# Kernel tuning notes

Hardware: AMD Instinct MI355X
Metric: run time of the kernel (lower is better)

The kernel has to match this reference:

```python
import jax, jax.numpy as jnp
import numpy as np
from jax import lax

REPLACE_PROB = 0.12
B, I, T = 16, 256, 8192


def setup_inputs() -> dict:
    key = jax.random.key(0)
    p = REPLACE_PROB
    s = 1.0 - 2.0 * p
    # probs[p2, p1, :] = P(x_t | x_{t-2}=p2, x_{t-1}=p1); all rows [p, s, p]
    # except [2,1] which disallows jitter value 0 (the '012' triplet) and renormalizes.
    probs = np.tile(np.array([p, s, p], dtype=np.float32), (3, 3, 1))
    probs[2, 1, :] = np.array([0.0, s / (p + s), p / (p + s)], dtype=np.float32)
    x = jax.random.normal(jax.random.fold_in(key, 1), (B, I, T), dtype=jnp.float32)
    return {"x": x, "probs": jnp.asarray(probs)}


def _gen_mindex(key, probs, n_batch, n_time):
    """Sample the (n_batch, n_time+1) jitter code sequence in alphabet {0,1,2}.
    mindex[:, 0:2] = 1, mindex[:, n_time] = 1, interior sampled by a
    2nd-order Markov scan: P(x_t | x_{t-2}, x_{t-1}) = probs[p2, p1]."""
    log_probs = jnp.log(probs)  # -inf for the zeroed entry is fine for categorical

    def one_seq(k):
        ks = jax.random.split(k, n_time - 2)

        def step(carry, kk):
            p2, p1 = carry
            j = jax.random.categorical(kk, log_probs[p2, p1]).astype(jnp.int32)
            return (p1, j), j

        _, js = lax.scan(step, (jnp.int32(1), jnp.int32(1)), ks)
        return js  # (n_time - 2,)

    js = jax.vmap(one_seq)(jax.random.split(key, n_batch))  # (B, T-2)
    ones2 = jnp.ones((n_batch, 2), jnp.int32)
    ones1 = jnp.ones((n_batch, 1), jnp.int32)
    return jnp.concatenate([ones2, js, ones1], axis=1)  # (B, T+1)


def reference(x, probs):
    n_batch, n_chan, n_time = x.shape
    mindex = _gen_mindex(jax.random.key(42), probs, n_batch, n_time)
    # torch code: mindex += (arange(T+1) - 2); y[b] = index_select(x[b], 1, mindex[b, 1:])
    # => source index for output position t is (t) + (jitter - 1), jitter in {0,1,2}
    idx = mindex[:, 1:] + (jnp.arange(n_time, dtype=jnp.int32) - 1)  # (B, T), in [0, T-1]
    return jnp.take_along_axis(x, idx[:, None, :], axis=2)  # (B, I, T)
```

## Files before the change

### kernel.cpp

```cpp
#include <hip/hip_runtime.h>
#include <stdint.h>

#define T_LEN 8192
#define NSTEP 8190
#define NB 16
#define NCH 256

__device__ __forceinline__ uint32_t rotl32(uint32_t v, int r) {
  return (v << r) | (v >> (32 - r));
}

__device__ __forceinline__ void tf2x32(uint32_t k0, uint32_t k1, uint32_t x0, uint32_t x1,
                                       uint32_t& o0, uint32_t& o1) {
  uint32_t ks2 = k0 ^ k1 ^ 0x1BD11BDAu;
  x0 += k0; x1 += k1;
#define RR(r) { x0 += x1; x1 = rotl32(x1, (r)); x1 ^= x0; }
  RR(13) RR(15) RR(26) RR(6)   x0 += k1;  x1 += ks2 + 1u;
  RR(17) RR(29) RR(16) RR(24)  x0 += ks2; x1 += k0 + 2u;
  RR(13) RR(15) RR(26) RR(6)   x0 += k0;  x1 += k1 + 3u;
  RR(17) RR(29) RR(16) RR(24)  x0 += k1;  x1 += ks2 + 4u;
  RR(13) RR(15) RR(26) RR(6)   x0 += ks2; x1 += k0 + 5u;
#undef RR
  o0 = x0; o1 = x1;
}

__global__ __launch_bounds__(256) void k_decide(const float* __restrict__ probs,
                                                uint8_t* __restrict__ dec) {
  int j = blockIdx.x * 256 + threadIdx.x;
  int b = blockIdx.y;
  if (j >= NSTEP) return;

  uint32_t kb0, kb1;
  tf2x32(0u, 42u, 0u, (uint32_t)b, kb0, kb1);
  uint32_t s0, s1;
  tf2x32(kb0, kb1, 0u, (uint32_t)j, s0, s1);

  uint32_t bits[3];
  {
    uint32_t y0, y1;
    tf2x32(s0, s1, 0u, 0u, y0, y1); bits[0] = y0 ^ y1;
    tf2x32(s0, s1, 0u, 1u, y0, y1); bits[1] = y0 ^ y1;
    tf2x32(s0, s1, 0u, 2u, y0, y1); bits[2] = y0 ^ y1;
  }

  double g[3];
#pragma unroll
  for (int c = 0; c < 3; ++c) {
    uint32_t k = bits[c] >> 9;
    float u = k ? (float)k * 0x1p-23f : 1.17549435e-38f;
    g[c] = -log(-log((double)u));
  }

  double lp = log((double)probs[0]);
  double ls = log((double)probs[1]);
  double l1 = log((double)probs[2 * 9 + 1 * 3 + 1]);
  double l2 = log((double)probs[2 * 9 + 1 * 3 + 2]);

  double v0 = lp + g[0], v1 = ls + g[1], v2 = lp + g[2];
  int n = 0; double best = v0;
  if (v1 > best) { n = 1; best = v1; }
  if (v2 > best) { n = 2; }
  int sp = (l1 + g[1] >= l2 + g[2]) ? 1 : 2;

  dec[b * NSTEP + j] = (uint8_t)(n | (sp << 2));
}

__device__ __forceinline__ uint64_t compose_map(uint64_t f, uint64_t g) {
  uint64_t r = 0;
#pragma unroll
  for (int st = 0; st < 9; ++st) {
    uint32_t fs = (uint32_t)((f >> (4 * st)) & 15u);
    uint32_t gs = (uint32_t)((g >> (4 * fs)) & 15u);
    r |= ((uint64_t)gs) << (4 * st);
  }
  return r;
}

__device__ __forceinline__ uint64_t shflup64(uint64_t v, int delta) {
  int lo = __shfl_up((int)(uint32_t)v, delta, 64);
  int hi = __shfl_up((int)(uint32_t)(v >> 32), delta, 64);
  return (((uint64_t)(uint32_t)hi) << 32) | (uint32_t)lo;
}

#define IDENT_MAP 0x876543210ull

__global__ __launch_bounds__(256) void k_scan(const uint8_t* __restrict__ dec,
                                              uint8_t* __restrict__ dbuf) {
  int b = blockIdx.x;
  int tid = threadIdx.x;
  int lane = tid & 63, wave = tid >> 6;
  int begin = tid * 32;
  const uint8_t* row = dec + b * NSTEP;

  uint64_t M = IDENT_MAP;
#pragma unroll
  for (int t = 0; t < 32; ++t) {
    int step = begin + t;
    if (step < NSTEP) {
      int d = row[step];
      uint32_t n = d & 3u, s = (d >> 2) & 3u;
      uint64_t Mn = 0;
#pragma unroll
      for (int st = 0; st < 9; ++st) {
        uint32_t u = (uint32_t)((M >> (4 * st)) & 15u);
        uint32_t div3 = (u * 11u) >> 5;
        uint32_t p1 = u - 3u * div3;
        uint32_t jj = (u == 7u) ? s : n;
        Mn |= ((uint64_t)(p1 * 3u + jj)) << (4 * st);
      }
      M = Mn;
    }
  }

  uint64_t I = M;
#pragma unroll
  for (int off = 1; off < 64; off <<= 1) {
    uint64_t Mp = shflup64(I, off);
    uint64_t c = compose_map(Mp, I);
    I = (lane >= off) ? c : I;
  }

  __shared__ uint64_t wmap[4];
  if (lane == 63) wmap[wave] = I;
  __syncthreads();

  uint64_t W = IDENT_MAP;
  for (int w = 0; w < wave; ++w) W = compose_map(W, wmap[w]);
  uint64_t E = shflup64(I, 1);
  if (lane == 0) E = IDENT_MAP;
  uint64_t X = compose_map(W, E);

  int state = (int)((X >> (4 * 4)) & 15u);

  uint8_t* orow = dbuf + b * T_LEN;
#pragma unroll
  for (int t = 0; t < 32; ++t) {
    int step = begin + t;
    if (step < NSTEP) {
      int d = row[step];
      uint32_t n = d & 3u, s = (d >> 2) & 3u;
      uint32_t jj = (state == 7) ? s : n;
      uint32_t div3 = ((uint32_t)state * 11u) >> 5;
      uint32_t p1 = (uint32_t)state - 3u * div3;
      state = (int)(p1 * 3u + jj);
      orow[step + 1] = (uint8_t)jj;
    }
  }
  if (tid == 0) { orow[0] = 1; orow[T_LEN - 1] = 1; }
}

typedef float f32x4 __attribute__((ext_vector_type(4)));

__global__ __launch_bounds__(256) void k_gather(const float* __restrict__ x,
                                                const uint8_t* __restrict__ dbuf,
                                                float* __restrict__ out) {
  __shared__ float shx[256];
  __shared__ float shw[256];

  const int bid = blockIdx.x;
  const int tc = bid & 7;
  const int i  = (bid >> 3) & 255;
  const int b  = bid >> 11;
  const int tid = threadIdx.x;
  const int t0 = tc * 1024 + tid * 4;

  const uchar4 du = *(const uchar4*)(dbuf + b * T_LEN + t0);
  const float* __restrict__ xr = x + ((size_t)(b * NCH + i)) * T_LEN;

  float4 v = *(const float4*)(xr + t0);

  float Le = 0.0f, Re = 0.0f;
  if (tid == 0)   Le = (t0 > 0) ? xr[t0 - 1] : 0.0f;
  if (tid == 255) Re = (t0 + 4 < T_LEN) ? xr[t0 + 4] : 0.0f;

  shx[tid] = v.x;
  shw[tid] = v.w;
  __syncthreads();

  const float L = (tid == 0)   ? Le : shw[tid - 1];
  const float R = (tid == 255) ? Re : shx[tid + 1];

  f32x4 o;
  o.x = (du.x == 0) ? L   : ((du.x == 1) ? v.x : v.y);
  o.y = (du.y == 0) ? v.x : ((du.y == 1) ? v.y : v.z);
  o.z = (du.z == 0) ? v.y : ((du.z == 1) ? v.z : v.w);
  o.w = (du.w == 0) ? v.z : ((du.w == 1) ? v.w : R);
  __builtin_nontemporal_store(o, (f32x4*)(out + ((size_t)(b * NCH + i)) * T_LEN + t0));
}

extern "C" void kernel_launch(void* const* d_in, const int* in_sizes, int n_in,
                              void* d_out, int out_size, void* d_ws, size_t ws_size,
                              hipStream_t stream) {
  const float* x = (const float*)d_in[0];
  const float* probs = (const float*)d_in[1];
  float* out = (float*)d_out;

  uint8_t* dec = (uint8_t*)d_ws;
  uint8_t* dbuf = (uint8_t*)d_ws + 131072;

  dim3 g1((NSTEP + 255) / 256, NB);
  k_decide<<<g1, 256, 0, stream>>>(probs, dec);

  k_scan<<<NB, 256, 0, stream>>>(dec, dbuf);

  k_gather<<<NB * NCH * 8, 256, 0, stream>>>(x, dbuf, out);
}
```

Measured before the change: 65.18 us.

## Use grid-stride persistent gather and load halo neighbors directly instead of LDS

The gather kernel now launches a fixed 2048 blocks that walk the whole output with a grid-stride loop, replacing the one-block-per-1024-element launch of 32768 blocks. The shared-memory exchange and __syncthreads used to get the neighbor elements are removed. Each thread instead loads its left and right neighbors straight from global memory, where they should usually hit in cache. This cuts block launch and barrier overhead but adds two scalar loads per thread and loop bookkeeping.

```diff
diff --git a/kernel.cpp b/kernel.cpp
--- a/kernel.cpp
+++ b/kernel.cpp
@@ -151,41 +151,36 @@
 
 typedef float f32x4 __attribute__((ext_vector_type(4)));
 
+#define GATHER_BLOCKS 2048
+
 __global__ __launch_bounds__(256) void k_gather(const float* __restrict__ x,
                                                 const uint8_t* __restrict__ dbuf,
                                                 float* __restrict__ out) {
-  __shared__ float shx[256];
-  __shared__ float shw[256];
-
-  const int bid = blockIdx.x;
-  const int tc = bid & 7;
-  const int i  = (bid >> 3) & 255;
-  const int b  = bid >> 11;
-  const int tid = threadIdx.x;
-  const int t0 = tc * 1024 + tid * 4;
-
-  const uchar4 du = *(const uchar4*)(dbuf + b * T_LEN + t0);
-  const float* __restrict__ xr = x + ((size_t)(b * NCH + i)) * T_LEN;
-
-  float4 v = *(const float4*)(xr + t0);
-
-  float Le = 0.0f, Re = 0.0f;
-  if (tid == 0)   Le = (t0 > 0) ? xr[t0 - 1] : 0.0f;
-  if (tid == 255) Re = (t0 + 4 < T_LEN) ? xr[t0 + 4] : 0.0f;
-
-  shx[tid] = v.x;
-  shw[tid] = v.w;
-  __syncthreads();
-
-  const float L = (tid == 0)   ? Le : shw[tid - 1];
-  const float R = (tid == 255) ? Re : shx[tid + 1];
-
-  f32x4 o;
-  o.x = (du.x == 0) ? L   : ((du.x == 1) ? v.x : v.y);
-  o.y = (du.y == 0) ? v.x : ((du.y == 1) ? v.y : v.z);
-  o.z = (du.z == 0) ? v.y : ((du.z == 1) ? v.z : v.w);
-  o.w = (du.w == 0) ? v.z : ((du.w == 1) ? v.w : R);
-  __builtin_nontemporal_store(o, (f32x4*)(out + ((size_t)(b * NCH + i)) * T_LEN + t0));
+  const size_t total = (size_t)NB * NCH * (T_LEN / 4);
+  const size_t stride = (size_t)GATHER_BLOCKS * 256;
+
+  for (size_t g = (size_t)blockIdx.x * 256 + threadIdx.x; g < total; g += stride) {
+    const int t4 = (int)(g & (T_LEN / 4 - 1));
+    const int i  = (int)((g >> 11) & (NCH - 1));
+    const int b  = (int)(g >> 19);
+    const int t0 = t4 * 4;
+
+    const uchar4 du = *(const uchar4*)(dbuf + b * T_LEN + t0);
+    const float* __restrict__ xr = x + ((size_t)(b * NCH + i)) * T_LEN;
+
+    const float4 v = *(const float4*)(xr + t0);
+    const int tl = (t0 == 0) ? 0 : t0 - 1;
+    const int tr = (t0 + 4 >= T_LEN) ? (T_LEN - 1) : t0 + 4;
+    const float L = xr[tl];
+    const float R = xr[tr];
+
+    f32x4 o;
+    o.x = (du.x == 0) ? L   : ((du.x == 1) ? v.x : v.y);
+    o.y = (du.y == 0) ? v.x : ((du.y == 1) ? v.y : v.z);
+    o.z = (du.z == 0) ? v.y : ((du.z == 1) ? v.z : v.w);
+    o.w = (du.w == 0) ? v.z : ((du.w == 1) ? v.w : R);
+    __builtin_nontemporal_store(o, (f32x4*)(out + ((size_t)(b * NCH + i)) * T_LEN + t0));
+  }
 }
 
 extern "C" void kernel_launch(void* const* d_in, const int* in_sizes, int n_in,
@@ -203,5 +198,5 @@
 
   k_scan<<<NB, 256, 0, stream>>>(dec, dbuf);
 
-  k_gather<<<NB * NCH * 8, 256, 0, stream>>>(x, dbuf, out);
-}
+  k_gather<<<GATHER_BLOCKS, 256, 0, stream>>>(x, dbuf, out);
+}
```

Result: no change. 66.11 us (+1.4%).

## Fuse decide and scan kernels using last-block-done atomic counter

Applied to the files above, without the earlier changes.

Merges the random-decision kernel and the per-batch Markov scan kernel into one launch. Each batch's 32 blocks increment an atomic counter, and the last block to finish runs the scan over that batch's decisions. This removes one kernel launch and its inter-kernel gap. It adds a memset of the counters, threadfences, and an atomic per block.

```diff
diff --git a/kernel.cpp b/kernel.cpp
--- a/kernel.cpp
+++ b/kernel.cpp
@@ -5,6 +5,7 @@
 #define NSTEP 8190
 #define NB 16
 #define NCH 256
+#define JBLKS 32
 
 __device__ __forceinline__ uint32_t rotl32(uint32_t v, int r) {
   return (v << r) | (v >> (32 - r));
@@ -24,47 +25,6 @@
   o0 = x0; o1 = x1;
 }
 
-__global__ __launch_bounds__(256) void k_decide(const float* __restrict__ probs,
-                                                uint8_t* __restrict__ dec) {
-  int j = blockIdx.x * 256 + threadIdx.x;
-  int b = blockIdx.y;
-  if (j >= NSTEP) return;
-
-  uint32_t kb0, kb1;
-  tf2x32(0u, 42u, 0u, (uint32_t)b, kb0, kb1);
-  uint32_t s0, s1;
-  tf2x32(kb0, kb1, 0u, (uint32_t)j, s0, s1);
-
-  uint32_t bits[3];
-  {
-    uint32_t y0, y1;
-    tf2x32(s0, s1, 0u, 0u, y0, y1); bits[0] = y0 ^ y1;
-    tf2x32(s0, s1, 0u, 1u, y0, y1); bits[1] = y0 ^ y1;
-    tf2x32(s0, s1, 0u, 2u, y0, y1); bits[2] = y0 ^ y1;
-  }
-
-  double g[3];
-#pragma unroll
-  for (int c = 0; c < 3; ++c) {
-    uint32_t k = bits[c] >> 9;
-    float u = k ? (float)k * 0x1p-23f : 1.17549435e-38f;
-    g[c] = -log(-log((double)u));
-  }
-
-  double lp = log((double)probs[0]);
-  double ls = log((double)probs[1]);
-  double l1 = log((double)probs[2 * 9 + 1 * 3 + 1]);
-  double l2 = log((double)probs[2 * 9 + 1 * 3 + 2]);
-
-  double v0 = lp + g[0], v1 = ls + g[1], v2 = lp + g[2];
-  int n = 0; double best = v0;
-  if (v1 > best) { n = 1; best = v1; }
-  if (v2 > best) { n = 2; }
-  int sp = (l1 + g[1] >= l2 + g[2]) ? 1 : 2;
-
-  dec[b * NSTEP + j] = (uint8_t)(n | (sp << 2));
-}
-
 __device__ __forceinline__ uint64_t compose_map(uint64_t f, uint64_t g) {
   uint64_t r = 0;
 #pragma unroll
@@ -84,12 +44,63 @@
 
 #define IDENT_MAP 0x876543210ull
 
-__global__ __launch_bounds__(256) void k_scan(const uint8_t* __restrict__ dec,
-                                              uint8_t* __restrict__ dbuf) {
-  int b = blockIdx.x;
-  int tid = threadIdx.x;
-  int lane = tid & 63, wave = tid >> 6;
-  int begin = tid * 32;
+__global__ __launch_bounds__(256) void k_prep(const float* __restrict__ probs,
+                                              uint8_t* __restrict__ dec,
+                                              uint8_t* __restrict__ dbuf,
+                                              uint32_t* __restrict__ cnt) {
+  const int tid = threadIdx.x;
+  const int b = blockIdx.y;
+  const int j = blockIdx.x * 256 + tid;
+
+  if (j < NSTEP) {
+    uint32_t kb0, kb1;
+    tf2x32(0u, 42u, 0u, (uint32_t)b, kb0, kb1);
+    uint32_t s0, s1;
+    tf2x32(kb0, kb1, 0u, (uint32_t)j, s0, s1);
+
+    uint32_t bits[3];
+    {
+      uint32_t y0, y1;
+      tf2x32(s0, s1, 0u, 0u, y0, y1); bits[0] = y0 ^ y1;
+      tf2x32(s0, s1, 0u, 1u, y0, y1); bits[1] = y0 ^ y1;
+      tf2x32(s0, s1, 0u, 2u, y0, y1); bits[2] = y0 ^ y1;
+    }
+
+    double g[3];
+#pragma unroll
+    for (int c = 0; c < 3; ++c) {
+      uint32_t k = bits[c] >> 9;
+      float u = k ? (float)k * 0x1p-23f : 1.17549435e-38f;
+      g[c] = -log(-log((double)u));
+    }
+
+    double lp = log((double)probs[0]);
+    double ls = log((double)probs[1]);
+    double l1 = log((double)probs[2 * 9 + 1 * 3 + 1]);
+    double l2 = log((double)probs[2 * 9 + 1 * 3 + 2]);
+
+    double v0 = lp + g[0], v1 = ls + g[1], v2 = lp + g[2];
+    int n = 0; double best = v0;
+    if (v1 > best) { n = 1; best = v1; }
+    if (v2 > best) { n = 2; }
+    int sp = (l1 + g[1] >= l2 + g[2]) ? 1 : 2;
+
+    dec[b * NSTEP + j] = (uint8_t)(n | (sp << 2));
+  }
+
+  __shared__ int do_scan;
+  __syncthreads();
+  if (tid == 0) {
+    __threadfence();
+    uint32_t old = atomicAdd(&cnt[b], 1u);
+    do_scan = (old == JBLKS - 1);
+  }
+  __syncthreads();
+  if (!do_scan) return;
+  __threadfence();
+
+  const int lane = tid & 63, wave = tid >> 6;
+  const int begin = tid * 32;
   const uint8_t* row = dec + b * NSTEP;
 
   uint64_t M = IDENT_MAP;
@@ -197,11 +208,12 @@
 
   uint8_t* dec = (uint8_t*)d_ws;
   uint8_t* dbuf = (uint8_t*)d_ws + 131072;
-
-  dim3 g1((NSTEP + 255) / 256, NB);
-  k_decide<<<g1, 256, 0, stream>>>(probs, dec);
-
-  k_scan<<<NB, 256, 0, stream>>>(dec, dbuf);
+  uint32_t* cnt = (uint32_t*)((char*)d_ws + 262144);
+
+  hipMemsetAsync(cnt, 0, NB * sizeof(uint32_t), stream);
+
+  dim3 g1(JBLKS, NB);
+  k_prep<<<g1, 256, 0, stream>>>(probs, dec, dbuf, cnt);
 
   k_gather<<<NB * NCH * 8, 256, 0, stream>>>(x, dbuf, out);
 }
```

Measured after the change: 86.71 us. +33.0%, slower.
